# Kernel optimization log

Measured on AMD Instinct MI355X. Metric: run time of the kernel, lower is better.

## Reference

```python
import jax, jax.numpy as jnp
import numpy as np

N = 131072  # time steps
D = 4       # SDE state dimension


def setup_inputs() -> dict:
    key = jax.random.key(0)
    k = jax.random.split(key, 6)
    F = 0.1 * jax.random.normal(k[0], (D, D), jnp.float32)  # only shape/dtype used by filter
    H = jnp.zeros((1, D), jnp.float32).at[0, 0].set(1.0)    # observe first state component
    P_inf = jnp.eye(D, dtype=jnp.float32)
    # stable per-step transitions: spectral radius ~0.9
    A_seq = 0.9 * jnp.eye(D, dtype=jnp.float32)[None] + 0.02 * jax.random.normal(k[1], (N, D, D), jnp.float32)
    # PSD process noise per step
    S = 0.05 * jax.random.normal(k[2], (N, D, D), jnp.float32)
    Q_seq = jnp.einsum('nij,nkj->nik', S, S) + 1e-3 * jnp.eye(D, dtype=jnp.float32)[None]
    residual = jax.random.normal(k[3], (N,), jnp.float32)   # y - mean_fn(times)
    mask = jnp.ones((N,), jnp.float32)                      # all steps observed
    R_seq = 0.1 + 0.05 * jax.random.uniform(k[4], (N,), jnp.float32)  # noise_var + floor
    return dict(F=F, H=H, P_inf=P_inf, A_seq=A_seq, Q_seq=Q_seq,
                residual=residual, mask=mask, R_seq=R_seq)


def _kalman_filter(F, H, P_inf, A_seq, Q_seq, residual, mask, R_seq):
    d = F.shape[0]
    eye = jnp.eye(d, dtype=F.dtype)
    h = H[0]  # (d,)
    log_2pi = jnp.log(2.0 * jnp.pi).astype(F.dtype)

    def step(carry, inputs):
        m, P = carry
        A, Q, r_n, mask_n, R_n = inputs
        m_pred = A @ m
        P_pred = A @ P @ A.T + Q
        P_pred = 0.5 * (P_pred + P_pred.T)
        Ph = P_pred @ h                 # (d,)
        S = h @ Ph + R_n                # innovation variance
        innov = r_n - h @ m_pred
        is_obs = mask_n == 1
        S_safe = jnp.where(is_obs, S, 1.0)
        K = jnp.where(is_obs, Ph / S_safe, jnp.zeros_like(Ph))
        m_new = m_pred + K * innov
        I_KH = eye - K[:, None] * h[None, :]
        P_new = I_KH @ P_pred @ I_KH.T + R_n * (K[:, None] * K[None, :])
        P_new = 0.5 * (P_new + P_new.T)
        ll = jnp.where(is_obs, -0.5 * (log_2pi + jnp.log(S_safe) + innov * innov / S_safe), 0.0)
        return (m_new, P_new), (m_pred, P_pred, m_new, P_new, ll)

    m0 = jnp.zeros(d, dtype=F.dtype)
    _, (m_pred_seq, P_pred_seq, m_filt_seq, P_filt_seq, ll_seq) = jax.lax.scan(
        step, (m0, P_inf), (A_seq, Q_seq, residual, mask, R_seq))
    return m_pred_seq, P_pred_seq, m_filt_seq, P_filt_seq, jnp.sum(ll_seq)


def _rts_smoother(m_pred_seq, P_pred_seq, m_filt_seq, P_filt_seq, A_seq):
    def step(carry, inputs):
        m_ns, P_ns = carry
        m_f, P_f, m_pn, P_pn, A_n = inputs
        J = jnp.linalg.solve(P_pn.T, A_n @ P_f.T).T
        m_s = m_f + J @ (m_ns - m_pn)
        P_s = P_f + J @ (P_ns - P_pn) @ J.T
        P_s = 0.5 * (P_s + P_s.T)
        return (m_s, P_s), (m_s, P_s)

    m_T = m_filt_seq[-1]
    P_T = P_filt_seq[-1]
    inputs = (m_filt_seq[:-1], P_filt_seq[:-1], m_pred_seq[1:], P_pred_seq[1:], A_seq[1:])
    _, (m_s, P_s) = jax.lax.scan(step, (m_T, P_T), inputs, reverse=True)
    return (jnp.concatenate([m_s, m_T[None]], axis=0),
            jnp.concatenate([P_s, P_T[None]], axis=0))


def reference(F, H, P_inf, A_seq, Q_seq, residual, mask, R_seq):
    m_pred, P_pred, m_filt, P_filt, log_marginal = _kalman_filter(
        F, H, P_inf, A_seq, Q_seq, residual, mask, R_seq)
    m_smooth, P_smooth = _rts_smoother(m_pred, P_pred, m_filt, P_filt, A_seq)
    h = H[0]
    means = m_smooth @ h                                   # (N,) observation-space means
    vars_ = jnp.einsum('i,nij,j->n', h, P_smooth, h)       # (N,) marginal variances
    return means, vars_, log_marginal
```

## Files before the change

### kernel.cpp

```cpp
#include <hip/hip_runtime.h>
#include <math.h>

#define NN 131072
#define WUP 32
#define TPB 256
#define NBLK (NN / TPB)
#define WINF (TPB + WUP + 1)
#define BTPB 320
#define SCAN_N (TPB + WUP)
#define LOG2PI 1.8378770664093453f

typedef __attribute__((ext_vector_type(2))) float f2;

__device__ float4 g_f[5][NN];
__device__ float4 g_J[4][NN];
__device__ float4 g_W0[NN];
__device__ float4 g_W1[NN];
__device__ float2 g_W2[NN];
__device__ float4 g_u[NN];
__device__ double g_llb[NBLK];

__device__ __forceinline__ f2 bc(float s) {
  f2 r = {s, s};
  return r;
}
#define PF(a, b, c) __builtin_elementwise_fma((a), (b), (c))

template <int E>
__device__ __forceinline__ void ldpk(const float4 (*s)[E], int w, f2* M) {
#pragma unroll
  for (int c = 0; c < 4; ++c) {
    float4 v = s[c][w];
    M[2 * c] = f2{v.x, v.y};
    M[2 * c + 1] = f2{v.z, v.w};
  }
}

__device__ __forceinline__ void sym_rows(const float4 t0, const float4 t1, const float2 t2,
                                         f2* M) {
  M[0] = f2{t0.x, t0.y};
  M[1] = f2{t0.z, t0.w};
  M[2] = f2{t0.y, t1.x};
  M[3] = f2{t1.y, t1.z};
  M[4] = f2{t0.z, t1.y};
  M[5] = f2{t1.w, t2.x};
  M[6] = f2{t0.w, t1.z};
  M[7] = f2{t2.x, t2.y};
}

__device__ __forceinline__ void kf_step_pk(const f2* __restrict__ AT, const f2* __restrict__ Q,
                                           float r, float mk, float R, f2* __restrict__ m,
                                           f2* __restrict__ P, float& Ss, float& innov,
                                           bool& obs) {
  float m0 = m[0][0], m1 = m[0][1], m2_ = m[1][0], m3 = m[1][1];
  f2 mp[2];
#pragma unroll
  for (int p = 0; p < 2; ++p) {
    f2 acc = AT[p] * bc(m0);
    acc = PF(bc(m1), AT[2 + p], acc);
    acc = PF(bc(m2_), AT[4 + p], acc);
    acc = PF(bc(m3), AT[6 + p], acc);
    mp[p] = acc;
  }

  f2 T[8];
#pragma unroll
  for (int i = 0; i < 4; ++i) {
    float a0 = AT[0 + (i >> 1)][i & 1];
    float a1 = AT[2 + (i >> 1)][i & 1];
    float a2 = AT[4 + (i >> 1)][i & 1];
    float a3 = AT[6 + (i >> 1)][i & 1];
#pragma unroll
    for (int p = 0; p < 2; ++p) {
      f2 acc = P[p] * bc(a0);
      acc = PF(bc(a1), P[2 + p], acc);
      acc = PF(bc(a2), P[4 + p], acc);
      acc = PF(bc(a3), P[6 + p], acc);
      T[2 * i + p] = acc;
    }
  }

  f2 Pp[8];
#pragma unroll
  for (int i = 0; i < 4; ++i) {
    float t0 = T[2 * i][0], t1 = T[2 * i][1], t2 = T[2 * i + 1][0], t3 = T[2 * i + 1][1];
#pragma unroll
    for (int p = 0; p < 2; ++p) {
      f2 acc = PF(bc(t0), AT[p], Q[2 * i + p]);
      acc = PF(bc(t1), AT[2 + p], acc);
      acc = PF(bc(t2), AT[4 + p], acc);
      acc = PF(bc(t3), AT[6 + p], acc);
      Pp[2 * i + p] = acc;
    }
  }

  float S = Pp[0][0] + R;
  innov = r - mp[0][0];
  obs = (mk == 1.0f);
  Ss = obs ? S : 1.0f;
  float kf = obs ? __builtin_amdgcn_rcpf(S) : 0.0f;
  f2 K[2] = {Pp[0] * bc(kf), Pp[1] * bc(kf)};
#pragma unroll
  for (int p = 0; p < 2; ++p) m[p] = PF(K[p], bc(innov), mp[p]);

#pragma unroll
  for (int i = 0; i < 4; ++i) {
    float Ki = K[i >> 1][i & 1];
#pragma unroll
    for (int p = 0; p < 2; ++p) P[2 * i + p] = PF(bc(-Ki), Pp[p], Pp[2 * i + p]);
  }
}

__device__ __forceinline__ void chol_solve_pk(const f2* __restrict__ S, const f2* __restrict__ T,
                                              f2* __restrict__ X) {
  float s00 = S[0][0];
  float s10 = S[2][0], s11 = S[2][1];
  float s20 = S[4][0], s21 = S[4][1], s22 = S[5][0];
  float s30 = S[6][0], s31 = S[6][1], s32 = S[7][0], s33 = S[7][1];
  float i00 = __builtin_amdgcn_rsqf(s00);
  float l10 = s10 * i00, l20 = s20 * i00, l30 = s30 * i00;
  float i11 = __builtin_amdgcn_rsqf(s11 - l10 * l10);
  float l21 = (s21 - l20 * l10) * i11;
  float l31 = (s31 - l30 * l10) * i11;
  float i22 = __builtin_amdgcn_rsqf(s22 - l20 * l20 - l21 * l21);
  float l32 = (s32 - l30 * l20 - l31 * l21) * i22;
  float i33 = __builtin_amdgcn_rsqf(s33 - l30 * l30 - l31 * l31 - l32 * l32);
#pragma unroll
  for (int c = 0; c < 4; ++c) {
    float t0 = T[0 + (c >> 1)][c & 1];
    float t1 = T[2 + (c >> 1)][c & 1];
    float t2 = T[4 + (c >> 1)][c & 1];
    float t3 = T[6 + (c >> 1)][c & 1];
    float y0 = t0 * i00;
    float y1 = (t1 - l10 * y0) * i11;
    float y2 = (t2 - l20 * y0 - l21 * y1) * i22;
    float y3 = (t3 - l30 * y0 - l31 * y1 - l32 * y2) * i33;
    float x3 = y3 * i33;
    float x2 = (y2 - l32 * x3) * i22;
    float x1 = (y1 - l21 * x2 - l31 * x3) * i11;
    float x0 = (y0 - l10 * x1 - l20 * x2 - l30 * x3) * i00;
    X[0 + (c >> 1)][c & 1] = x0;
    X[2 + (c >> 1)][c & 1] = x1;
    X[4 + (c >> 1)][c & 1] = x2;
    X[6 + (c >> 1)][c & 1] = x3;
  }
}

__device__ __forceinline__ void make_record_pk(int n, const f2* __restrict__ m,
                                               const f2* __restrict__ P,
                                               const f2* __restrict__ AT,
                                               const f2* __restrict__ Q) {
  float m0 = m[0][0], m1 = m[0][1], m2_ = m[1][0], m3 = m[1][1];
  f2 pm[2];
#pragma unroll
  for (int p = 0; p < 2; ++p) {
    f2 acc = AT[p] * bc(m0);
    acc = PF(bc(m1), AT[2 + p], acc);
    acc = PF(bc(m2_), AT[4 + p], acc);
    acc = PF(bc(m3), AT[6 + p], acc);
    pm[p] = acc;
  }

  f2 T[8];
#pragma unroll
  for (int i = 0; i < 4; ++i) {
    float a0 = AT[0 + (i >> 1)][i & 1];
    float a1 = AT[2 + (i >> 1)][i & 1];
    float a2 = AT[4 + (i >> 1)][i & 1];
    float a3 = AT[6 + (i >> 1)][i & 1];
#pragma unroll
    for (int p = 0; p < 2; ++p) {
      f2 acc = P[p] * bc(a0);
      acc = PF(bc(a1), P[2 + p], acc);
      acc = PF(bc(a2), P[4 + p], acc);
      acc = PF(bc(a3), P[6 + p], acc);
      T[2 * i + p] = acc;
    }
  }

  f2 Ppn[8];
#pragma unroll
  for (int i = 0; i < 4; ++i) {
    float t0 = T[2 * i][0], t1 = T[2 * i][1], t2 = T[2 * i + 1][0], t3 = T[2 * i + 1][1];
#pragma unroll
    for (int p = 0; p < 2; ++p) {
      f2 acc = PF(bc(t0), AT[p], Q[2 * i + p]);
      acc = PF(bc(t1), AT[2 + p], acc);
      acc = PF(bc(t2), AT[4 + p], acc);
      acc = PF(bc(t3), AT[6 + p], acc);
      Ppn[2 * i + p] = acc;
    }
  }

  f2 X[8];
  chol_solve_pk(Ppn, T, X);

  float p0 = pm[0][0], p1 = pm[0][1], p2 = pm[1][0], p3 = pm[1][1];
  f2 u[2];
#pragma unroll
  for (int p = 0; p < 2; ++p) {
    f2 acc = X[p] * bc(p0);
    acc = PF(bc(p1), X[2 + p], acc);
    acc = PF(bc(p2), X[4 + p], acc);
    acc = PF(bc(p3), X[6 + p], acc);
    u[p] = m[p] - acc;
  }

  f2 Jp[8];
#pragma unroll
  for (int i = 0; i < 4; ++i) {
    float x0 = X[0 + (i >> 1)][i & 1];
    float x1 = X[2 + (i >> 1)][i & 1];
    float x2 = X[4 + (i >> 1)][i & 1];
    float x3 = X[6 + (i >> 1)][i & 1];
#pragma unroll
    for (int p = 0; p < 2; ++p) {
      f2 acc = Ppn[p] * bc(x0);
      acc = PF(bc(x1), Ppn[2 + p], acc);
      acc = PF(bc(x2), Ppn[4 + p], acc);
      acc = PF(bc(x3), Ppn[6 + p], acc);
      Jp[2 * i + p] = acc;
    }
  }
  f2 W[8];
#pragma unroll
  for (int i = 0; i < 4; ++i) {
    float j0 = Jp[2 * i][0], j1 = Jp[2 * i][1], j2 = Jp[2 * i + 1][0], j3 = Jp[2 * i + 1][1];
#pragma unroll
    for (int p = 0; p < 2; ++p) {
      f2 acc = X[p] * bc(j0);
      acc = PF(bc(j1), X[2 + p], acc);
      acc = PF(bc(j2), X[4 + p], acc);
      acc = PF(bc(j3), X[6 + p], acc);
      W[2 * i + p] = P[2 * i + p] - acc;
    }
  }

#pragma unroll
  for (int i = 0; i < 4; ++i)
    g_J[i][n] = make_float4(X[2 * i][0], X[2 * i][1], X[2 * i + 1][0], X[2 * i + 1][1]);
  g_W0[n] = make_float4(W[0][0], W[0][1], W[1][0], W[1][1]);
  g_W1[n] = make_float4(W[2][1], W[3][0], W[3][1], W[5][0]);
  g_W2[n] = make_float2(W[5][1], W[7][1]);
  g_u[n] = make_float4(u[0][0], u[0][1], u[1][0], u[1][1]);
}

__device__ __forceinline__ void compose_pk(f2* __restrict__ X, f2* __restrict__ W,
                                           f2* __restrict__ u, const f2* __restrict__ Xb,
                                           const f2* __restrict__ Wb,
                                           const f2* __restrict__ ub) {
  f2 Xc[8];
#pragma unroll
  for (int i = 0; i < 4; ++i) {
    float b0 = Xb[2 * i][0], b1 = Xb[2 * i][1], b2 = Xb[2 * i + 1][0], b3 = Xb[2 * i + 1][1];
#pragma unroll
    for (int p = 0; p < 2; ++p) {
      f2 acc = X[p] * bc(b0);
      acc = PF(bc(b1), X[2 + p], acc);
      acc = PF(bc(b2), X[4 + p], acc);
      acc = PF(bc(b3), X[6 + p], acc);
      Xc[2 * i + p] = acc;
    }
  }
  float ub0 = ub[0][0], ub1 = ub[0][1], ub2 = ub[1][0], ub3 = ub[1][1];
  f2 uc[2];
#pragma unroll
  for (int p = 0; p < 2; ++p) {
    f2 acc = PF(bc(ub0), X[p], u[p]);
    acc = PF(bc(ub1), X[2 + p], acc);
    acc = PF(bc(ub2), X[4 + p], acc);
    acc = PF(bc(ub3), X[6 + p], acc);
    uc[p] = acc;
  }
  f2 V[8];
#pragma unroll
  for (int q = 0; q < 4; ++q) {
    float w0 = Wb[2 * q][0], w1 = Wb[2 * q][1], w2 = Wb[2 * q + 1][0], w3 = Wb[2 * q + 1][1];
#pragma unroll
    for (int p = 0; p < 2; ++p) {
      f2 acc = X[p] * bc(w0);
      acc = PF(bc(w1), X[2 + p], acc);
      acc = PF(bc(w2), X[4 + p], acc);
      acc = PF(bc(w3), X[6 + p], acc);
      V[2 * q + p] = acc;
    }
  }
#pragma unroll
  for (int i = 0; i < 4; ++i) {
    float x0 = X[0 + (i >> 1)][i & 1];
    float x1 = X[2 + (i >> 1)][i & 1];
    float x2 = X[4 + (i >> 1)][i & 1];
    float x3 = X[6 + (i >> 1)][i & 1];
    f2 w0, w1;
    {
      f2 acc = PF(bc(x0), V[0], W[2 * i + 0]);
      acc = PF(bc(x1), V[2], acc);
      acc = PF(bc(x2), V[4], acc);
      acc = PF(bc(x3), V[6], acc);
      w0 = acc;
    }
    {
      f2 acc = PF(bc(x0), V[1], W[2 * i + 1]);
      acc = PF(bc(x1), V[3], acc);
      acc = PF(bc(x2), V[5], acc);
      acc = PF(bc(x3), V[7], acc);
      w1 = acc;
    }
    W[2 * i + 0] = w0;
    W[2 * i + 1] = w1;
  }
#pragma unroll
  for (int i = 0; i < 8; ++i) X[i] = Xc[i];
  u[0] = uc[0];
  u[1] = uc[1];
}

__global__ __launch_bounds__(TPB, 1) void fwd_kernel(const float* __restrict__ P_inf,
                                                     const float* __restrict__ A_seq,
                                                     const float* __restrict__ Q_seq,
                                                     const float* __restrict__ residual,
                                                     const float* __restrict__ mask,
                                                     const float* __restrict__ R_seq) {
  __shared__ float4 sAT[4][WINF];
  __shared__ float4 sQ0[WINF], sQ1[WINF];
  __shared__ float2 sQ2[WINF];
  __shared__ float4 sRM[WINF];
  __shared__ double swl[TPB / 64];

  const int B = blockIdx.x * TPB;
  const int base = B - WUP;
  const float4* Af4 = (const float4*)A_seq;
  const float4* Qf4 = (const float4*)Q_seq;
  for (int f = threadIdx.x; f < WINF * 4; f += TPB) {
    int w = f >> 2, c = f & 3;
    int k = base + w;
    k = k < 0 ? 0 : (k > NN - 1 ? NN - 1 : k);
    float4 rowA = Af4[(size_t)k * 4 + c];
    ((float*)&sAT[0][w])[c] = rowA.x;
    ((float*)&sAT[1][w])[c] = rowA.y;
    ((float*)&sAT[2][w])[c] = rowA.z;
    ((float*)&sAT[3][w])[c] = rowA.w;
    float4 rowQ = Qf4[(size_t)k * 4 + c];
    if (c == 0) {
      sQ0[w] = rowQ;
    } else if (c == 1) {
      sQ1[w].x = rowQ.y;
      sQ1[w].y = rowQ.z;
      sQ1[w].z = rowQ.w;
    } else if (c == 2) {
      sQ1[w].w = rowQ.z;
      sQ2[w].x = rowQ.w;
    } else {
      sQ2[w].y = rowQ.w;
    }
  }
  for (int w = threadIdx.x; w < WINF; w += TPB) {
    int k = base + w;
    k = k < 0 ? 0 : (k > NN - 1 ? NN - 1 : k);
    sRM[w] = make_float4(residual[k], R_seq[k], mask[k], 0.f);
  }
  __syncthreads();

  const int t = threadIdx.x;
  const int n = B + t;
  int s0 = n - WUP;
  if (s0 < 0) s0 = 0;

  f2 m[2] = {f2{0.f, 0.f}, f2{0.f, 0.f}};
  f2 P[8];
#pragma unroll
  for (int i = 0; i < 4; ++i) {
    P[2 * i] = f2{P_inf[i * 4 + 0], P_inf[i * 4 + 1]};
    P[2 * i + 1] = f2{P_inf[i * 4 + 2], P_inf[i * 4 + 3]};
  }

  float Ss = 1.f, innov = 0.f;
  bool obs = false;
#pragma unroll 2
  for (int k = s0; k <= n; ++k) {
    int w = k - base;
    f2 AT[8], Q[8];
    ldpk<WINF>(sAT, w, AT);
    sym_rows(sQ0[w], sQ1[w], sQ2[w], Q);
    float4 rm = sRM[w];
    kf_step_pk(AT, Q, rm.x, rm.z, rm.y, m, P, Ss, innov, obs);
  }

#pragma unroll
  for (int c = 0; c < 4; ++c)
    g_f[c][n] = make_float4(P[2 * c][0], P[2 * c][1], P[2 * c + 1][0], P[2 * c + 1][1]);
  g_f[4][n] = make_float4(m[0][0], m[0][1], m[1][0], m[1][1]);

  if (n < NN - 1) {
    int w = n + 1 - base;
    f2 AT[8], Q[8];
    ldpk<WINF>(sAT, w, AT);
    sym_rows(sQ0[w], sQ1[w], sQ2[w], Q);
    make_record_pk(n, m, P, AT, Q);
  }

  double llv = obs ? (double)(-0.5f * (LOG2PI + logf(Ss) + innov * innov / Ss)) : 0.0;
#pragma unroll
  for (int o = 32; o > 0; o >>= 1) llv += __shfl_down(llv, o, 64);
  if ((t & 63) == 0) swl[t >> 6] = llv;
  __syncthreads();
  if (t == 0) g_llb[blockIdx.x] = swl[0] + swl[1] + swl[2] + swl[3];
}

__global__ __launch_bounds__(BTPB, 1) void bwd_kernel(float* __restrict__ out) {
  __shared__ float4 pJ[2][4][SCAN_N];
  __shared__ float4 pW0[2][SCAN_N], pW1[2][SCAN_N];
  __shared__ float2 pW2[2][SCAN_N];
  __shared__ float4 pu[2][SCAN_N];
  __shared__ double swb[BTPB / 64];

  const int B = blockIdx.x * TPB;
  const int t = threadIdx.x;
  const bool own = (t < SCAN_N);
  const int k = B + t;

  const int ii = (B + SCAN_N <= NN - 1) ? (B + SCAN_N) : (NN - 1);
  f2 Pi[8], mi[2];
#pragma unroll
  for (int c = 0; c < 4; ++c) {
    float4 v = g_f[c][ii];
    Pi[2 * c] = f2{v.x, v.y};
    Pi[2 * c + 1] = f2{v.z, v.w};
  }
  {
    float4 v = g_f[4][ii];
    mi[0] = f2{v.x, v.y};
    mi[1] = f2{v.z, v.w};
  }

  f2 X[8], W[8], u[2];
  if (own && k < NN - 1) {
#pragma unroll
    for (int c = 0; c < 4; ++c) {
      float4 v = g_J[c][k];
      X[2 * c] = f2{v.x, v.y};
      X[2 * c + 1] = f2{v.z, v.w};
    }
    sym_rows(g_W0[k], g_W1[k], g_W2[k], W);
    float4 v = g_u[k];
    u[0] = f2{v.x, v.y};
    u[1] = f2{v.z, v.w};
  } else {
    X[0] = f2{1.f, 0.f}; X[1] = f2{0.f, 0.f};
    X[2] = f2{0.f, 1.f}; X[3] = f2{0.f, 0.f};
    X[4] = f2{0.f, 0.f}; X[5] = f2{1.f, 0.f};
    X[6] = f2{0.f, 0.f}; X[7] = f2{0.f, 1.f};
#pragma unroll
    for (int i = 0; i < 8; ++i) W[i] = f2{0.f, 0.f};
    u[0] = f2{0.f, 0.f};
    u[1] = f2{0.f, 0.f};
  }

  int buf = 0;
  for (int d = 1; d < SCAN_N; d <<= 2) {
    if (own) {
#pragma unroll
      for (int c = 0; c < 4; ++c)
        pJ[buf][c][t] = make_float4(X[2 * c][0], X[2 * c][1], X[2 * c + 1][0], X[2 * c + 1][1]);
      pW0[buf][t] = make_float4(W[0][0], W[0][1], W[1][0], W[1][1]);
      pW1[buf][t] = make_float4(W[2][1], W[3][0], W[3][1], W[5][0]);
      pW2[buf][t] = make_float2(W[5][1], W[7][1]);
      pu[buf][t] = make_float4(u[0][0], u[0][1], u[1][0], u[1][1]);
    }
    __syncthreads();
    if (own) {
#pragma unroll
      for (int j = 1; j <= 3; ++j) {
        const int s = t + j * d;
        if (s < SCAN_N) {
          f2 Xb[8], Wb[8], ub[2];
#pragma unroll
          for (int c = 0; c < 4; ++c) {
            float4 v = pJ[buf][c][s];
            Xb[2 * c] = f2{v.x, v.y};
            Xb[2 * c + 1] = f2{v.z, v.w};
          }
          sym_rows(pW0[buf][s], pW1[buf][s], pW2[buf][s], Wb);
          float4 v = pu[buf][s];
          ub[0] = f2{v.x, v.y};
          ub[1] = f2{v.z, v.w};
          compose_pk(X, W, u, Xb, Wb, ub);
        }
      }
    }
    buf ^= 1;
  }

  if (t < TPB) {
    float x00 = X[0][0], x01 = X[2][0], x02 = X[4][0], x03 = X[6][0];
    float mean = u[0][0] + x00 * mi[0][0] + x01 * mi[0][1] + x02 * mi[1][0] + x03 * mi[1][1];
    float t0 = Pi[0][0] * x00 + Pi[0][1] * x01 + Pi[1][0] * x02 + Pi[1][1] * x03;
    float t1 = Pi[2][0] * x00 + Pi[2][1] * x01 + Pi[3][0] * x02 + Pi[3][1] * x03;
    float t2 = Pi[4][0] * x00 + Pi[4][1] * x01 + Pi[5][0] * x02 + Pi[5][1] * x03;
    float t3 = Pi[6][0] * x00 + Pi[6][1] * x01 + Pi[7][0] * x02 + Pi[7][1] * x03;
    float var = W[0][0] + x00 * t0 + x01 * t1 + x02 * t2 + x03 * t3;
    out[B + t] = mean;
    out[NN + B + t] = var;
  }

  if (blockIdx.x == 0) {
    double acc = 0.0;
    for (int i = t; i < NBLK; i += BTPB) acc += g_llb[i];
#pragma unroll
    for (int o = 32; o > 0; o >>= 1) acc += __shfl_down(acc, o, 64);
    if ((t & 63) == 0) swb[t >> 6] = acc;
    __syncthreads();
    if (t == 0) out[2 * NN] = (float)(swb[0] + swb[1] + swb[2] + swb[3] + swb[4]);
  }
}

extern "C" void kernel_launch(void* const* d_in, const int* in_sizes, int n_in, void* d_out,
                              int out_size, void* d_ws, size_t ws_size, hipStream_t stream) {
  const float* P_inf = (const float*)d_in[2];
  const float* A_seq = (const float*)d_in[3];
  const float* Q_seq = (const float*)d_in[4];
  const float* residual = (const float*)d_in[5];
  const float* mask = (const float*)d_in[6];
  const float* R_seq = (const float*)d_in[7];
  float* out = (float*)d_out;

  fwd_kernel<<<NBLK, TPB, 0, stream>>>(P_inf, A_seq, Q_seq, residual, mask, R_seq);
  bwd_kernel<<<NBLK, BTPB, 0, stream>>>(out);
}
```

Before: 120.8 us.

## Replace shared-memory radix-4 backward scan with wavefront shuffle scan plus cross-wave combine

The backward kernel's block-wide suffix scan over affine smoother elements is restructured. It drops the shared-memory radix-4 Hillis-Steele scan, which needed a __syncthreads per stage. Instead each 64-lane wavefront runs a shuffle-based suffix scan, then each thread composes with the aggregates of the later wavefronts through a small shared array. This removes most LDS traffic and block barriers, at the cost of more scan steps (radix 2) and many shuffles per step for 18 f2 values.

```diff
diff --git a/kernel.cpp b/kernel.cpp
--- a/kernel.cpp
+++ b/kernel.cpp
@@ -25,6 +25,13 @@
   return r;
 }
 #define PF(a, b, c) __builtin_elementwise_fma((a), (b), (c))
+
+__device__ __forceinline__ f2 shfl_dn(f2 v, int d) {
+  f2 r;
+  r[0] = __shfl_down(v[0], d, 64);
+  r[1] = __shfl_down(v[1], d, 64);
+  return r;
+}
 
 template <int E>
 __device__ __forceinline__ void ldpk(const float4 (*s)[E], int w, f2* M) {
@@ -408,15 +415,15 @@
 }
 
 __global__ __launch_bounds__(BTPB, 1) void bwd_kernel(float* __restrict__ out) {
-  __shared__ float4 pJ[2][4][SCAN_N];
-  __shared__ float4 pW0[2][SCAN_N], pW1[2][SCAN_N];
-  __shared__ float2 pW2[2][SCAN_N];
-  __shared__ float4 pu[2][SCAN_N];
+  __shared__ f2 aX[5][8];
+  __shared__ f2 aW[5][8];
+  __shared__ f2 au[5][2];
   __shared__ double swb[BTPB / 64];
 
   const int B = blockIdx.x * TPB;
   const int t = threadIdx.x;
-  const bool own = (t < SCAN_N);
+  const int lane = t & 63;
+  const int wv = t >> 6;
   const int k = B + t;
 
   const int ii = (B + SCAN_N <= NN - 1) ? (B + SCAN_N) : (NN - 1);
@@ -434,7 +441,7 @@
   }
 
   f2 X[8], W[8], u[2];
-  if (own && k < NN - 1) {
+  if (t < SCAN_N && k < NN - 1) {
 #pragma unroll
     for (int c = 0; c < 4; ++c) {
       float4 v = g_J[c][k];
@@ -456,39 +463,39 @@
     u[1] = f2{0.f, 0.f};
   }
 
-  int buf = 0;
-  for (int d = 1; d < SCAN_N; d <<= 2) {
-    if (own) {
-#pragma unroll
-      for (int c = 0; c < 4; ++c)
-        pJ[buf][c][t] = make_float4(X[2 * c][0], X[2 * c][1], X[2 * c + 1][0], X[2 * c + 1][1]);
-      pW0[buf][t] = make_float4(W[0][0], W[0][1], W[1][0], W[1][1]);
-      pW1[buf][t] = make_float4(W[2][1], W[3][0], W[3][1], W[5][0]);
-      pW2[buf][t] = make_float2(W[5][1], W[7][1]);
-      pu[buf][t] = make_float4(u[0][0], u[0][1], u[1][0], u[1][1]);
-    }
-    __syncthreads();
-    if (own) {
-#pragma unroll
-      for (int j = 1; j <= 3; ++j) {
-        const int s = t + j * d;
-        if (s < SCAN_N) {
-          f2 Xb[8], Wb[8], ub[2];
-#pragma unroll
-          for (int c = 0; c < 4; ++c) {
-            float4 v = pJ[buf][c][s];
-            Xb[2 * c] = f2{v.x, v.y};
-            Xb[2 * c + 1] = f2{v.z, v.w};
-          }
-          sym_rows(pW0[buf][s], pW1[buf][s], pW2[buf][s], Wb);
-          float4 v = pu[buf][s];
-          ub[0] = f2{v.x, v.y};
-          ub[1] = f2{v.z, v.w};
-          compose_pk(X, W, u, Xb, Wb, ub);
-        }
-      }
-    }
-    buf ^= 1;
+#pragma unroll
+  for (int d = 1; d < 64; d <<= 1) {
+    f2 Xb[8], Wb[8], ub[2];
+#pragma unroll
+    for (int i = 0; i < 8; ++i) {
+      Xb[i] = shfl_dn(X[i], d);
+      Wb[i] = shfl_dn(W[i], d);
+    }
+    ub[0] = shfl_dn(u[0], d);
+    ub[1] = shfl_dn(u[1], d);
+    if (lane + d < 64) compose_pk(X, W, u, Xb, Wb, ub);
+  }
+
+  if (lane == 0) {
+#pragma unroll
+    for (int i = 0; i < 8; ++i) {
+      aX[wv][i] = X[i];
+      aW[wv][i] = W[i];
+    }
+    au[wv][0] = u[0];
+    au[wv][1] = u[1];
+  }
+  __syncthreads();
+  for (int j = wv + 1; j < 5; ++j) {
+    f2 Xb[8], Wb[8], ub[2];
+#pragma unroll
+    for (int i = 0; i < 8; ++i) {
+      Xb[i] = aX[j][i];
+      Wb[i] = aW[j][i];
+    }
+    ub[0] = au[j][0];
+    ub[1] = au[j][1];
+    compose_pk(X, W, u, Xb, Wb, ub);
   }
 
   if (t < TPB) {
```

Measured after the change: 120.9 us. No clear change (+0.0%).
